# Optimization experiments

Measured on AMD Instinct MI355X. Metric: run time of the kernel, lower is better.

## Reference

```python
import jax, jax.numpy as jnp
import numpy as np

N = 100000
F = 512
D = 128
E = 1600000

def setup_inputs() -> dict:
    key = jax.random.key(0)
    k1, k2, k3, k4, k5 = jax.random.split(key, 5)
    feature = jax.random.normal(k1, (N, F), dtype=jnp.float32)
    W = jax.random.normal(k2, (F, D), dtype=jnp.float32) * (1.0 / np.sqrt(D))
    bias = jax.random.normal(k3, (D,), dtype=jnp.float32) * (1.0 / np.sqrt(D))
    edge_vals = jax.random.uniform(k4, (E,), dtype=jnp.float32)
    edge_index = jax.random.randint(k5, (2, E), 0, N, dtype=jnp.int32)
    return {"feature": feature, "W": W, "bias": bias,
            "edge_vals": edge_vals, "edge_index": edge_index}

def reference(feature, W, bias, edge_vals, edge_index):
    # support = relu(feature @ W)                          [N, D]
    support = jax.nn.relu(feature @ W)
    row, col = edge_index[0], edge_index[1]
    # spmm(adj, support): gather source rows, scale, scatter-add to dest rows
    msgs = edge_vals[:, None] * support[col]               # [E, D]
    agg = jax.ops.segment_sum(msgs, row, num_segments=feature.shape[0])
    # adj_low = adj + I  ->  identity contributes +support; then + bias
    return agg + support + bias
```

## Files before the change

kernel.cpp:

```cpp
#include <hip/hip_runtime.h>
#include <hip/hip_bf16.h>

typedef __attribute__((ext_vector_type(8))) __bf16 bf16x8;
typedef __attribute__((ext_vector_type(4))) float f32x4;

#define F_DIM 512
#define D_DIM 128
#define RPB 128
#define MAXBUK 1024
#define BIN_CHUNK 8192
#define CAPMAX 3072

__device__ __forceinline__ unsigned short f32_to_bf16_rn(float x) {
    union { float f; unsigned u; } v; v.f = x;
    unsigned u = v.u;
    unsigned rounded = u + 0x7fffu + ((u >> 16) & 1u);
    return (unsigned short)(rounded >> 16);
}
__device__ __forceinline__ float bf16_to_f32(unsigned short u) {
    return __uint_as_float((unsigned)u << 16);
}

__global__ void prep_kernel(const float* __restrict__ W, unsigned short* __restrict__ Wt) {
    int idx = blockIdx.x * 256 + threadIdx.x;
    int n = idx >> 9;
    int k = idx & 511;
    Wt[idx] = f32_to_bf16_rn(W[k * D_DIM + n]);
}

__global__ __launch_bounds__(256) void fused_gemm_bin(
    const float* __restrict__ A, const unsigned short* __restrict__ Bt,
    unsigned short* __restrict__ Sb, int Nrows,
    const int* __restrict__ ei, const float* __restrict__ ev,
    int* __restrict__ cursor, uint2* __restrict__ ecv, int E, int nbuk,
    int cap, int binBlocks)
{
    __shared__ __align__(16) char smem[30720];
    const int tid = threadIdx.x;

    if ((int)blockIdx.x < binBlocks) {
        int* cnt = (int*)smem;
        int* bas = (int*)(smem + 4096);
        const int e0 = blockIdx.x * BIN_CHUNK;
        const int e1 = min(e0 + BIN_CHUNK, E);

        for (int i = tid; i < nbuk; i += 256) cnt[i] = 0;
        __syncthreads();
        for (int e = e0 + tid; e < e1; e += 256)
            atomicAdd(&cnt[ei[e] >> 7], 1);
        __syncthreads();
        for (int i = tid; i < nbuk; i += 256) {
            int c = cnt[i];
            bas[i] = c ? (i * cap + atomicAdd(&cursor[i], c)) : 0;
            cnt[i] = 0;
        }
        __syncthreads();
        for (int e = e0 + tid; e < e1; e += 256) {
            int r = ei[e];
            int b = r >> 7;
            int slot = atomicAdd(&cnt[b], 1);
            uint2 cv;
            cv.x = ((unsigned)ei[E + e] << 7) | (unsigned)(r & 127);
            cv.y = __float_as_uint(ev[e]);
            ecv[(size_t)bas[b] + slot] = cv;
        }
        return;
    }

    unsigned short* Al = (unsigned short*)smem;
    unsigned short* Bl = (unsigned short*)(smem + 10240);

    const int gb   = blockIdx.x - binBlocks;
    const int wave = tid >> 6;
    const int lane = tid & 63;
    const int g    = lane >> 4;
    const int r16  = lane & 15;
    const int m0   = gb * 64;

    const int sar = tid >> 2;
    const int skq = tid & 3;
    int arow = m0 + sar;
    if (arow >= Nrows) arow = Nrows - 1;
    const float* aptr = A + (size_t)arow * F_DIM + skq * 8;
    const int awoff = sar * 40 + skq * 8;

    const int sbr = tid >> 1;
    const int skh = tid & 1;
    const unsigned short* bptr = Bt + (size_t)sbr * F_DIM + skh * 16;
    const int bwoff = sbr * 40 + skh * 16;

    float4 ar0, ar1;
    uint4  br0, br1;

    auto loadAB = [&](int ks) {
        const float4* pa = (const float4*)(aptr + ks * 32);
        ar0 = pa[0]; ar1 = pa[1];
        const uint4* pb = (const uint4*)(bptr + ks * 32);
        br0 = pb[0]; br1 = pb[1];
    };
    auto storeAB = [&](int buf) {
        union { uint4 q; __bf16 h[8]; } u;
        u.h[0]=(__bf16)ar0.x; u.h[1]=(__bf16)ar0.y; u.h[2]=(__bf16)ar0.z; u.h[3]=(__bf16)ar0.w;
        u.h[4]=(__bf16)ar1.x; u.h[5]=(__bf16)ar1.y; u.h[6]=(__bf16)ar1.z; u.h[7]=(__bf16)ar1.w;
        *(uint4*)&Al[buf * 2560 + awoff] = u.q;
        unsigned short* bw = &Bl[buf * 5120 + bwoff];
        *(uint4*)bw       = br0;
        *(uint4*)(bw + 8) = br1;
    };

    f32x4 acc[8];
#pragma unroll
    for (int j = 0; j < 8; ++j) acc[j] = (f32x4)0.0f;

    loadAB(0);
    storeAB(0);
    __syncthreads();

#pragma unroll
    for (int ks = 0; ks < 16; ++ks) {
        const int cur = ks & 1;
        if (ks < 15) loadAB(ks + 1);

        const unsigned short* Ab = Al + cur * 2560;
        const unsigned short* Bb = Bl + cur * 5120;
        bf16x8 af = *(const bf16x8*)&Ab[(wave * 16 + r16) * 40 + g * 8];
#pragma unroll
        for (int nf = 0; nf < 8; ++nf) {
            bf16x8 bf = *(const bf16x8*)&Bb[(nf * 16 + r16) * 40 + g * 8];
            acc[nf] = __builtin_amdgcn_mfma_f32_16x16x32_bf16(af, bf, acc[nf], 0, 0, 0);
        }

        if (ks < 15) storeAB(cur ^ 1);
        __syncthreads();
    }

#pragma unroll
    for (int nf = 0; nf < 8; ++nf) {
#pragma unroll
        for (int r = 0; r < 4; ++r) {
            int row = m0 + wave * 16 + g * 4 + r;
            if (row < Nrows) {
                float v = acc[nf][r];
                Sb[(size_t)row * D_DIM + nf * 16 + r16] = f32_to_bf16_rn(v > 0.f ? v : 0.f);
            }
        }
    }
}

__global__ __launch_bounds__(512) void sortaccum_kernel(
    const uint2* __restrict__ ecv, const int* __restrict__ cursor,
    const unsigned short* __restrict__ Sb, const float* __restrict__ bias,
    float* __restrict__ out, int Nrows, int cap)
{
    __shared__ uint2 raw[CAPMAX];
    __shared__ uint2 srt[CAPMAX];
    __shared__ int cnt[RPB];
    __shared__ int base[RPB];
    __shared__ int scur[RPB];

    const int tid = threadIdx.x;
    const int b   = blockIdx.x;
    const int beg = b * cap;
    int n = cursor[b];
    if (n > cap) n = cap;

    if (tid < RPB) cnt[tid] = 0;
    __syncthreads();
    for (int i = tid; i < n; i += 512) {
        uint2 cv = ecv[beg + i];
        raw[i] = cv;
        atomicAdd(&cnt[cv.x & 127], 1);
    }
    __syncthreads();
    if (tid < 64) {
        int carry = 0;
#pragma unroll
        for (int c = 0; c < 2; ++c) {
            int idx = c * 64 + tid;
            int v = cnt[idx];
            int orig = v;
            for (int d = 1; d < 64; d <<= 1) {
                int t = __shfl_up(v, d, 64);
                if (tid >= d) v += t;
            }
            int excl = carry + v - orig;
            base[idx] = excl;
            scur[idx] = excl;
            carry += __shfl(v, 63, 64);
        }
    }
    __syncthreads();
    for (int i = tid; i < n; i += 512) {
        uint2 cv = raw[i];
        int slot = atomicAdd(&scur[cv.x & 127], 1);
        srt[slot] = cv;
    }
    __syncthreads();

    const int wv   = tid >> 6;
    const int lane = tid & 63;
    const int c2   = lane * 2;
    const int r0g  = b * RPB;

#define GATHER(J) \
    uint2 cv##J = srt[i + J]; \
    ushort2 sv##J = *(const ushort2*)&Sb[(size_t)(cv##J.x >> 7) * D_DIM + c2];

#define ACCUM(J) { \
    float v = __uint_as_float(cv##J.y); \
    float sel = ((int)(cv##J.x & 127) == rl0) ? 1.f : 0.f; \
    float px = v * bf16_to_f32(sv##J.x); \
    float py = v * bf16_to_f32(sv##J.y); \
    ax0 += sel * px; ay0 += sel * py; \
    ax1 += px - sel * px; ay1 += py - sel * py; }

    for (int rr = 0; rr < 16; rr += 2) {
        const int rl0 = wv * 16 + rr;
        const int s  = base[rl0];
        const int e  = s + cnt[rl0] + cnt[rl0 + 1];

        float ax0 = 0.f, ay0 = 0.f, ax1 = 0.f, ay1 = 0.f;
        int i = s;
        for (; i + 7 < e; i += 8) {
            GATHER(0) GATHER(1) GATHER(2) GATHER(3)
            GATHER(4) GATHER(5) GATHER(6) GATHER(7)
            ACCUM(0) ACCUM(1) ACCUM(2) ACCUM(3)
            ACCUM(4) ACCUM(5) ACCUM(6) ACCUM(7)
        }
        for (; i < e; ++i) {
            GATHER(0)
            ACCUM(0)
        }

        int row0 = r0g + rl0;
        if (row0 < Nrows) {
            ushort2 so = *(const ushort2*)&Sb[(size_t)row0 * D_DIM + c2];
            float2 bv = *(const float2*)&bias[c2];
            float2 o;
            o.x = ax0 + bf16_to_f32(so.x) + bv.x;
            o.y = ay0 + bf16_to_f32(so.y) + bv.y;
            *(float2*)&out[(size_t)row0 * D_DIM + c2] = o;
        }
        int row1 = row0 + 1;
        if (row1 < Nrows) {
            ushort2 so = *(const ushort2*)&Sb[(size_t)row1 * D_DIM + c2];
            float2 bv = *(const float2*)&bias[c2];
            float2 o;
            o.x = ax1 + bf16_to_f32(so.x) + bv.x;
            o.y = ay1 + bf16_to_f32(so.y) + bv.y;
            *(float2*)&out[(size_t)row1 * D_DIM + c2] = o;
        }
    }
#undef GATHER
#undef ACCUM
}

extern "C" void kernel_launch(void* const* d_in, const int* in_sizes, int n_in,
                              void* d_out, int out_size, void* d_ws, size_t ws_size,
                              hipStream_t stream) {
    const float* feature = (const float*)d_in[0];
    const float* W       = (const float*)d_in[1];
    const float* bias    = (const float*)d_in[2];
    const float* ev      = (const float*)d_in[3];
    const int*   ei      = (const int*)d_in[4];
    float* out = (float*)d_out;

    const int N = in_sizes[0] / F_DIM;
    const int E = in_sizes[3];
    const int nbuk = (N + RPB - 1) / RPB;
    int cap = (E + nbuk - 1) / nbuk;
    cap = cap + cap / 4 + 256;
    if (cap > CAPMAX) cap = CAPMAX;

    char* ws = (char*)d_ws;
    size_t cur = 0;
    auto alloc = [&](size_t bytes) -> void* {
        void* p = ws + cur;
        cur = (cur + bytes + 255) & ~(size_t)255;
        return p;
    };
    unsigned short* Sb     = (unsigned short*)alloc((size_t)N * D_DIM * 2);
    unsigned short* Wt     = (unsigned short*)alloc((size_t)D_DIM * F_DIM * 2);
    int*            cursor = (int*)alloc((size_t)nbuk * 4);
    uint2*          ecv    = (uint2*)alloc(((size_t)nbuk * cap + BIN_CHUNK) * 8);
    (void)ws_size;

    const int binBlocks  = (E + BIN_CHUNK - 1) / BIN_CHUNK;
    const int gemmBlocks = (N + 63) / 64;

    hipMemsetAsync(cursor, 0, (size_t)nbuk * 4, stream);
    prep_kernel<<<256, 256, 0, stream>>>(W, Wt);
    fused_gemm_bin<<<binBlocks + gemmBlocks, 256, 0, stream>>>(
        feature, Wt, Sb, N, ei, ev, cursor, ecv, E, nbuk, cap, binBlocks);
    sortaccum_kernel<<<nbuk, 512, 0, stream>>>(ecv, cursor, Sb, bias, out, N, cap);
}
```

Measured before the change: 199.0 us.

## Deepen GEMM global prefetch to two stages and use lgkm-only barriers

The feature-times-weight GEMM loop now keeps two register sets of prefetched A/B tiles, loading two k-steps ahead instead of one. `__syncthreads` is replaced with an LDS-only wait (`s_waitcnt lgkmcnt(0)`) plus `s_barrier`. This lets global loads stay in flight across barriers instead of forcing a full memory drain each iteration. The aim is to hide more HBM latency on the streaming fp32 feature reads, at the cost of more registers, which may reduce occupancy.

Result: no change. 198.7 us (-0.2%).

```diff
diff --git a/kernel.cpp b/kernel.cpp
--- a/kernel.cpp
+++ b/kernel.cpp
@@ -89,40 +89,39 @@
     const unsigned short* bptr = Bt + (size_t)sbr * F_DIM + skh * 16;
     const int bwoff = sbr * 40 + skh * 16;
 
-    float4 ar0, ar1;
-    uint4  br0, br1;
-
-    auto loadAB = [&](int ks) {
-        const float4* pa = (const float4*)(aptr + ks * 32);
-        ar0 = pa[0]; ar1 = pa[1];
-        const uint4* pb = (const uint4*)(bptr + ks * 32);
-        br0 = pb[0]; br1 = pb[1];
-    };
-    auto storeAB = [&](int buf) {
-        union { uint4 q; __bf16 h[8]; } u;
-        u.h[0]=(__bf16)ar0.x; u.h[1]=(__bf16)ar0.y; u.h[2]=(__bf16)ar0.z; u.h[3]=(__bf16)ar0.w;
-        u.h[4]=(__bf16)ar1.x; u.h[5]=(__bf16)ar1.y; u.h[6]=(__bf16)ar1.z; u.h[7]=(__bf16)ar1.w;
-        *(uint4*)&Al[buf * 2560 + awoff] = u.q;
-        unsigned short* bw = &Bl[buf * 5120 + bwoff];
-        *(uint4*)bw       = br0;
-        *(uint4*)(bw + 8) = br1;
-    };
+    float4 a0_0, a0_1; uint4 b0_0, b0_1;
+    float4 a1_0, a1_1; uint4 b1_0, b1_1;
+
+#define LOADSET(aR0, aR1, bR0, bR1, ks) { \
+    const float4* pa = (const float4*)(aptr + (ks) * 32); \
+    aR0 = pa[0]; aR1 = pa[1]; \
+    const uint4* pb = (const uint4*)(bptr + (ks) * 32); \
+    bR0 = pb[0]; bR1 = pb[1]; }
+
+#define STORESET(aR0, aR1, bR0, bR1, buf) { \
+    union { uint4 q; __bf16 h[8]; } u; \
+    u.h[0]=(__bf16)aR0.x; u.h[1]=(__bf16)aR0.y; u.h[2]=(__bf16)aR0.z; u.h[3]=(__bf16)aR0.w; \
+    u.h[4]=(__bf16)aR1.x; u.h[5]=(__bf16)aR1.y; u.h[6]=(__bf16)aR1.z; u.h[7]=(__bf16)aR1.w; \
+    *(uint4*)&Al[(buf) * 2560 + awoff] = u.q; \
+    unsigned short* bw = &Bl[(buf) * 5120 + bwoff]; \
+    *(uint4*)bw       = bR0; \
+    *(uint4*)(bw + 8) = bR1; }
 
     f32x4 acc[8];
 #pragma unroll
     for (int j = 0; j < 8; ++j) acc[j] = (f32x4)0.0f;
 
-    loadAB(0);
-    storeAB(0);
-    __syncthreads();
+    LOADSET(a0_0, a0_1, b0_0, b0_1, 0);
+    STORESET(a0_0, a0_1, b0_0, b0_1, 0);
+    LOADSET(a1_0, a1_1, b1_0, b1_1, 1);
+    LOADSET(a0_0, a0_1, b0_0, b0_1, 2);
+    asm volatile("s_waitcnt lgkmcnt(0)" ::: "memory");
+    __builtin_amdgcn_s_barrier();
 
 #pragma unroll
     for (int ks = 0; ks < 16; ++ks) {
-        const int cur = ks & 1;
-        if (ks < 15) loadAB(ks + 1);
-
-        const unsigned short* Ab = Al + cur * 2560;
-        const unsigned short* Bb = Bl + cur * 5120;
+        const unsigned short* Ab = Al + (ks & 1) * 2560;
+        const unsigned short* Bb = Bl + (ks & 1) * 5120;
         bf16x8 af = *(const bf16x8*)&Ab[(wave * 16 + r16) * 40 + g * 8];
 #pragma unroll
         for (int nf = 0; nf < 8; ++nf) {
@@ -130,9 +129,20 @@
             acc[nf] = __builtin_amdgcn_mfma_f32_16x16x32_bf16(af, bf, acc[nf], 0, 0, 0);
         }
 
-        if (ks < 15) storeAB(cur ^ 1);
-        __syncthreads();
-    }
+        if (ks < 15) {
+            if ((ks & 1) == 0) {
+                STORESET(a1_0, a1_1, b1_0, b1_1, (ks + 1) & 1);
+                if (ks + 3 < 16) LOADSET(a1_0, a1_1, b1_0, b1_1, ks + 3);
+            } else {
+                STORESET(a0_0, a0_1, b0_0, b0_1, (ks + 1) & 1);
+                if (ks + 3 < 16) LOADSET(a0_0, a0_1, b0_0, b0_1, ks + 3);
+            }
+        }
+        asm volatile("s_waitcnt lgkmcnt(0)" ::: "memory");
+        __builtin_amdgcn_s_barrier();
+    }
+#undef LOADSET
+#undef STORESET
 
 #pragma unroll
     for (int nf = 0; nf < 8; ++nf) {
```

## Restructure GEMM into two half-K stages with swizzled LDS and register-streamed B

Applied to the files above, without the earlier changes.

The GEMM mainloop moves from 16 double-buffered K-steps of 32 to two half-K stages of 256. Each thread prefetches 64 floats of A into registers, converts them to bf16 and writes them into an XOR-swizzled LDS tile. The B fragments now come straight from global memory (L2) into registers, prefetched one step ahead, instead of being staged through shared memory. This cuts the barriers from 16 to a few and removes LDS traffic for B, in exchange for much higher register pressure (64 floats of A plus 16 bf16x8 of B fragments), which may lower occupancy.

Measured after the change: 257.4 us. +29.4%, slower.

```diff
diff --git a/kernel.cpp b/kernel.cpp
--- a/kernel.cpp
+++ b/kernel.cpp
@@ -35,7 +35,7 @@
     int* __restrict__ cursor, uint2* __restrict__ ecv, int E, int nbuk,
     int cap, int binBlocks)
 {
-    __shared__ __align__(16) char smem[30720];
+    __shared__ __align__(16) char smem[32768];
     const int tid = threadIdx.x;
 
     if ((int)blockIdx.x < binBlocks) {
@@ -67,8 +67,7 @@
         return;
     }
 
-    unsigned short* Al = (unsigned short*)smem;
-    unsigned short* Bl = (unsigned short*)(smem + 10240);
+    unsigned short* Aw = (unsigned short*)smem;
 
     const int gb   = blockIdx.x - binBlocks;
     const int wave = tid >> 6;
@@ -77,61 +76,80 @@
     const int r16  = lane & 15;
     const int m0   = gb * 64;
 
-    const int sar = tid >> 2;
-    const int skq = tid & 3;
-    int arow = m0 + sar;
+    const int rt = tid >> 2;
+    const int qt = tid & 3;
+    int arow = m0 + rt;
     if (arow >= Nrows) arow = Nrows - 1;
-    const float* aptr = A + (size_t)arow * F_DIM + skq * 8;
-    const int awoff = sar * 40 + skq * 8;
-
-    const int sbr = tid >> 1;
-    const int skh = tid & 1;
-    const unsigned short* bptr = Bt + (size_t)sbr * F_DIM + skh * 16;
-    const int bwoff = sbr * 40 + skh * 16;
-
-    float4 ar0, ar1;
-    uint4  br0, br1;
-
-    auto loadAB = [&](int ks) {
-        const float4* pa = (const float4*)(aptr + ks * 32);
-        ar0 = pa[0]; ar1 = pa[1];
-        const uint4* pb = (const uint4*)(bptr + ks * 32);
-        br0 = pb[0]; br1 = pb[1];
+    const float* aptr = A + (size_t)arow * F_DIM + qt * 64;
+
+    float4 sa[16];
+    auto loadStage = [&](int s) {
+#pragma unroll
+        for (int i = 0; i < 16; ++i)
+            sa[i] = *(const float4*)(aptr + s * 256 + i * 4);
     };
-    auto storeAB = [&](int buf) {
-        union { uint4 q; __bf16 h[8]; } u;
-        u.h[0]=(__bf16)ar0.x; u.h[1]=(__bf16)ar0.y; u.h[2]=(__bf16)ar0.z; u.h[3]=(__bf16)ar0.w;
-        u.h[4]=(__bf16)ar1.x; u.h[5]=(__bf16)ar1.y; u.h[6]=(__bf16)ar1.z; u.h[7]=(__bf16)ar1.w;
-        *(uint4*)&Al[buf * 2560 + awoff] = u.q;
-        unsigned short* bw = &Bl[buf * 5120 + bwoff];
-        *(uint4*)bw       = br0;
-        *(uint4*)(bw + 8) = br1;
+    auto storeStage = [&]() {
+#pragma unroll
+        for (int j = 0; j < 8; ++j) {
+            union { uint4 q; __bf16 h[8]; } u;
+            u.h[0]=(__bf16)sa[2*j].x;   u.h[1]=(__bf16)sa[2*j].y;
+            u.h[2]=(__bf16)sa[2*j].z;   u.h[3]=(__bf16)sa[2*j].w;
+            u.h[4]=(__bf16)sa[2*j+1].x; u.h[5]=(__bf16)sa[2*j+1].y;
+            u.h[6]=(__bf16)sa[2*j+1].z; u.h[7]=(__bf16)sa[2*j+1].w;
+            int c = qt * 8 + j;
+            *(uint4*)(Aw + (size_t)rt * 256 + ((c ^ (rt & 15)) << 3)) = u.q;
+        }
     };
 
+    const unsigned short* bb = Bt + (size_t)r16 * F_DIM + g * 8;
+    bf16x8 bcur[8], bnext[8];
+    auto loadB = [&](bf16x8* dst, int kg) {
+#pragma unroll
+        for (int nf = 0; nf < 8; ++nf)
+            dst[nf] = *(const bf16x8*)(bb + (size_t)nf * 16 * F_DIM + kg * 32);
+    };
+
+    const unsigned short* Ar = Aw + (size_t)(wave * 16 + r16) * 256;
+
     f32x4 acc[8];
 #pragma unroll
     for (int j = 0; j < 8; ++j) acc[j] = (f32x4)0.0f;
 
-    loadAB(0);
-    storeAB(0);
-    __syncthreads();
-
-#pragma unroll
-    for (int ks = 0; ks < 16; ++ks) {
-        const int cur = ks & 1;
-        if (ks < 15) loadAB(ks + 1);
-
-        const unsigned short* Ab = Al + cur * 2560;
-        const unsigned short* Bb = Bl + cur * 5120;
-        bf16x8 af = *(const bf16x8*)&Ab[(wave * 16 + r16) * 40 + g * 8];
-#pragma unroll
-        for (int nf = 0; nf < 8; ++nf) {
-            bf16x8 bf = *(const bf16x8*)&Bb[(nf * 16 + r16) * 40 + g * 8];
-            acc[nf] = __builtin_amdgcn_mfma_f32_16x16x32_bf16(af, bf, acc[nf], 0, 0, 0);
-        }
-
-        if (ks < 15) storeAB(cur ^ 1);
-        __syncthreads();
+    loadStage(0);
+    loadB(bcur, 0);
+    storeStage();
+    asm volatile("s_waitcnt lgkmcnt(0)" ::: "memory");
+    __builtin_amdgcn_s_barrier();
+
+#pragma unroll
+    for (int ks = 0; ks < 8; ++ks) {
+        if (ks == 3) loadStage(1);
+        loadB(bnext, ks + 1);
+        bf16x8 af = *(const bf16x8*)(Ar + (((ks * 4 + g) ^ r16) << 3));
+#pragma unroll
+        for (int nf = 0; nf < 8; ++nf)
+            acc[nf] = __builtin_amdgcn_mfma_f32_16x16x32_bf16(af, bcur[nf], acc[nf], 0, 0, 0);
+#pragma unroll
+        for (int nf = 0; nf < 8; ++nf) bcur[nf] = bnext[nf];
+    }
+    asm volatile("s_waitcnt lgkmcnt(0)" ::: "memory");
+    __builtin_amdgcn_s_barrier();
+    storeStage();
+    asm volatile("s_waitcnt lgkmcnt(0)" ::: "memory");
+    __builtin_amdgcn_s_barrier();
+
+#pragma unroll
+    for (int ks = 0; ks < 8; ++ks) {
+        const int kg = 8 + ks;
+        if (kg < 15) loadB(bnext, kg + 1);
+        bf16x8 af = *(const bf16x8*)(Ar + (((ks * 4 + g) ^ r16) << 3));
+#pragma unroll
+        for (int nf = 0; nf < 8; ++nf)
+            acc[nf] = __builtin_amdgcn_mfma_f32_16x16x32_bf16(af, bcur[nf], acc[nf], 0, 0, 0);
+        if (kg < 15) {
+#pragma unroll
+            for (int nf = 0; nf < 8; ++nf) bcur[nf] = bnext[nf];
+        }
     }
 
 #pragma unroll
```

## Pre-convert features to bf16 and stream A via global_load_lds in GEMM

Applied to the files above, without the earlier changes.

Splits the fused GEMM/bin kernel: a combined prep kernel now bins edges, transposes W, and converts the whole feature matrix to bf16 in a separate buffer. The GEMM then loads A tiles directly to LDS with global_load_lds and a swizzled layout, and reads B fragments straight from global memory instead of staging them in LDS. This aims to simplify the GEMM inner loop and cut LDS traffic, but adds a full extra write and read of an N x F bf16 copy of the features.

After: 310.5 us. +56.0%, slower.

```diff
diff --git a/kernel.cpp b/kernel.cpp
--- a/kernel.cpp
+++ b/kernel.cpp
@@ -7,7 +7,6 @@
 #define F_DIM 512
 #define D_DIM 128
 #define RPB 128
-#define MAXBUK 1024
 #define BIN_CHUNK 8192
 #define CAPMAX 3072
 
@@ -20,28 +19,27 @@
 __device__ __forceinline__ float bf16_to_f32(unsigned short u) {
     return __uint_as_float((unsigned)u << 16);
 }
-
-__global__ void prep_kernel(const float* __restrict__ W, unsigned short* __restrict__ Wt) {
-    int idx = blockIdx.x * 256 + threadIdx.x;
-    int n = idx >> 9;
-    int k = idx & 511;
-    Wt[idx] = f32_to_bf16_rn(W[k * D_DIM + n]);
-}
-
-__global__ __launch_bounds__(256) void fused_gemm_bin(
-    const float* __restrict__ A, const unsigned short* __restrict__ Bt,
-    unsigned short* __restrict__ Sb, int Nrows,
+__device__ __forceinline__ void gload_lds16(const void* g, void* l) {
+    __builtin_amdgcn_global_load_lds(
+        (const __attribute__((address_space(1))) void*)g,
+        (__attribute__((address_space(3))) void*)l, 16, 0, 0);
+}
+
+__global__ __launch_bounds__(256) void prep_bin_conv(
+    const float* __restrict__ A, unsigned short* __restrict__ Af,
+    const float* __restrict__ W, unsigned short* __restrict__ Wt,
     const int* __restrict__ ei, const float* __restrict__ ev,
-    int* __restrict__ cursor, uint2* __restrict__ ecv, int E, int nbuk,
-    int cap, int binBlocks)
+    int* __restrict__ cursor, uint2* __restrict__ ecv,
+    int E, int nbuk, int cap, int binBlocks, int convBlocks, long long nA)
 {
-    __shared__ __align__(16) char smem[30720];
+    __shared__ int smem[2048];
     const int tid = threadIdx.x;
-
-    if ((int)blockIdx.x < binBlocks) {
-        int* cnt = (int*)smem;
-        int* bas = (int*)(smem + 4096);
-        const int e0 = blockIdx.x * BIN_CHUNK;
+    const int b = blockIdx.x;
+
+    if (b < binBlocks) {
+        int* cnt = smem;
+        int* bas = smem + 1024;
+        const int e0 = b * BIN_CHUNK;
         const int e1 = min(e0 + BIN_CHUNK, E);
 
         for (int i = tid; i < nbuk; i += 256) cnt[i] = 0;
@@ -57,80 +55,84 @@
         __syncthreads();
         for (int e = e0 + tid; e < e1; e += 256) {
             int r = ei[e];
-            int b = r >> 7;
-            int slot = atomicAdd(&cnt[b], 1);
+            int bk = r >> 7;
+            int slot = atomicAdd(&cnt[bk], 1);
             uint2 cv;
             cv.x = ((unsigned)ei[E + e] << 7) | (unsigned)(r & 127);
             cv.y = __float_as_uint(ev[e]);
-            ecv[(size_t)bas[b] + slot] = cv;
-        }
-        return;
-    }
-
-    unsigned short* Al = (unsigned short*)smem;
-    unsigned short* Bl = (unsigned short*)(smem + 10240);
-
-    const int gb   = blockIdx.x - binBlocks;
+            ecv[(size_t)bas[bk] + slot] = cv;
+        }
+    } else if (b < binBlocks + 256) {
+        int idx = (b - binBlocks) * 256 + tid;
+        int n = idx >> 9;
+        int k = idx & 511;
+        Wt[idx] = f32_to_bf16_rn(W[k * D_DIM + n]);
+    } else {
+        long long i = ((long long)(b - binBlocks - 256) * 256 + tid) * 8;
+        const long long stride = (long long)convBlocks * 2048;
+        for (; i < nA; i += stride) {
+            float4 v0 = *(const float4*)&A[i];
+            float4 v1 = *(const float4*)&A[i + 4];
+            union { uint4 q; unsigned short h[8]; } u;
+            u.h[0] = f32_to_bf16_rn(v0.x); u.h[1] = f32_to_bf16_rn(v0.y);
+            u.h[2] = f32_to_bf16_rn(v0.z); u.h[3] = f32_to_bf16_rn(v0.w);
+            u.h[4] = f32_to_bf16_rn(v1.x); u.h[5] = f32_to_bf16_rn(v1.y);
+            u.h[6] = f32_to_bf16_rn(v1.z); u.h[7] = f32_to_bf16_rn(v1.w);
+            *(uint4*)&Af[i] = u.q;
+        }
+    }
+}
+
+__global__ __launch_bounds__(256) void gemm_bf16_gll(
+    const unsigned short* __restrict__ Af,
+    const unsigned short* __restrict__ Bt,
+    unsigned short* __restrict__ Sb,
+    int Nrows)
+{
+    __shared__ unsigned short Al[2 * 64 * 32];
+    const int tid  = threadIdx.x;
     const int wave = tid >> 6;
     const int lane = tid & 63;
     const int g    = lane >> 4;
     const int r16  = lane & 15;
-    const int m0   = gb * 64;
-
-    const int sar = tid >> 2;
-    const int skq = tid & 3;
-    int arow = m0 + sar;
+    const int m0   = blockIdx.x * 64;
+
+    const int srow = wave * 16 + (lane >> 2);
+    const int skey = (srow >> 1) & 3;
+    const int cg   = (lane & 3) ^ skey;
+    int arow = m0 + srow;
     if (arow >= Nrows) arow = Nrows - 1;
-    const float* aptr = A + (size_t)arow * F_DIM + skq * 8;
-    const int awoff = sar * 40 + skq * 8;
-
-    const int sbr = tid >> 1;
-    const int skh = tid & 1;
-    const unsigned short* bptr = Bt + (size_t)sbr * F_DIM + skh * 16;
-    const int bwoff = sbr * 40 + skh * 16;
-
-    float4 ar0, ar1;
-    uint4  br0, br1;
-
-    auto loadAB = [&](int ks) {
-        const float4* pa = (const float4*)(aptr + ks * 32);
-        ar0 = pa[0]; ar1 = pa[1];
-        const uint4* pb = (const uint4*)(bptr + ks * 32);
-        br0 = pb[0]; br1 = pb[1];
-    };
-    auto storeAB = [&](int buf) {
-        union { uint4 q; __bf16 h[8]; } u;
-        u.h[0]=(__bf16)ar0.x; u.h[1]=(__bf16)ar0.y; u.h[2]=(__bf16)ar0.z; u.h[3]=(__bf16)ar0.w;
-        u.h[4]=(__bf16)ar1.x; u.h[5]=(__bf16)ar1.y; u.h[6]=(__bf16)ar1.z; u.h[7]=(__bf16)ar1.w;
-        *(uint4*)&Al[buf * 2560 + awoff] = u.q;
-        unsigned short* bw = &Bl[buf * 5120 + bwoff];
-        *(uint4*)bw       = br0;
-        *(uint4*)(bw + 8) = br1;
-    };
+    const unsigned short* gsrc = Af + (size_t)arow * F_DIM + cg * 8;
+    const int ldsbase = wave * 1024;
 
     f32x4 acc[8];
 #pragma unroll
     for (int j = 0; j < 8; ++j) acc[j] = (f32x4)0.0f;
 
-    loadAB(0);
-    storeAB(0);
-    __syncthreads();
+    gload_lds16(gsrc, (char*)Al + ldsbase);
+    __syncthreads();
+
+    const int myrow = wave * 16 + r16;
+    const int rkey  = (myrow >> 1) & 3;
+    const int aoff  = myrow * 64 + ((g ^ rkey) << 4);
 
 #pragma unroll
     for (int ks = 0; ks < 16; ++ks) {
         const int cur = ks & 1;
-        if (ks < 15) loadAB(ks + 1);
-
-        const unsigned short* Ab = Al + cur * 2560;
-        const unsigned short* Bb = Bl + cur * 5120;
-        bf16x8 af = *(const bf16x8*)&Ab[(wave * 16 + r16) * 40 + g * 8];
-#pragma unroll
-        for (int nf = 0; nf < 8; ++nf) {
-            bf16x8 bf = *(const bf16x8*)&Bb[(nf * 16 + r16) * 40 + g * 8];
-            acc[nf] = __builtin_amdgcn_mfma_f32_16x16x32_bf16(af, bf, acc[nf], 0, 0, 0);
-        }
-
-        if (ks < 15) storeAB(cur ^ 1);
+        if (ks < 15)
+            gload_lds16(gsrc + (ks + 1) * 32, (char*)Al + (cur ^ 1) * 4096 + ldsbase);
+
+        bf16x8 bfr[8];
+#pragma unroll
+        for (int nf = 0; nf < 8; ++nf)
+            bfr[nf] = *(const bf16x8*)&Bt[(size_t)(nf * 16 + r16) * F_DIM + ks * 32 + g * 8];
+
+        bf16x8 af = *(const bf16x8*)((const char*)Al + cur * 4096 + aoff);
+
+#pragma unroll
+        for (int nf = 0; nf < 8; ++nf)
+            acc[nf] = __builtin_amdgcn_mfma_f32_16x16x32_bf16(af, bfr[nf], acc[nf], 0, 0, 0);
+
         __syncthreads();
     }
 
@@ -283,14 +285,17 @@
     unsigned short* Wt     = (unsigned short*)alloc((size_t)D_DIM * F_DIM * 2);
     int*            cursor = (int*)alloc((size_t)nbuk * 4);
     uint2*          ecv    = (uint2*)alloc(((size_t)nbuk * cap + BIN_CHUNK) * 8);
+    unsigned short* Af     = (unsigned short*)alloc((size_t)N * F_DIM * 2);
     (void)ws_size;
 
     const int binBlocks  = (E + BIN_CHUNK - 1) / BIN_CHUNK;
-    const int gemmBlocks = (N + 63) / 64;
+    const int convBlocks = 2048 - binBlocks - 256;
+    const long long nA   = (long long)N * F_DIM;
 
     hipMemsetAsync(cursor, 0, (size_t)nbuk * 4, stream);
-    prep_kernel<<<256, 256, 0, stream>>>(W, Wt);
-    fused_gemm_bin<<<binBlocks + gemmBlocks, 256, 0, stream>>>(
-        feature, Wt, Sb, N, ei, ev, cursor, ecv, E, nbuk, cap, binBlocks);
+    prep_bin_conv<<<2048, 256, 0, stream>>>(feature, Af, W, Wt, ei, ev,
+                                            cursor, ecv, E, nbuk, cap,
+                                            binBlocks, convBlocks, nA);
+    gemm_bf16_gll<<<(N + 63) / 64, 256, 0, stream>>>(Af, Wt, Sb, N);
     sortaccum_kernel<<<nbuk, 512, 0, stream>>>(ecv, cursor, Sb, bias, out, N, cap);
 }
```
